# Performance work log

Measured on AMD Instinct MI355X. Metric: run time of the kernel, lower is better.

Reference implementation:

```python
import jax, jax.numpy as jnp
import numpy as np

B, N_IN, D, A, O = 2048, 2048, 1024, 4, 2048
C = 1 << A              # LUT channels per detector (sequence_length == 1)
N_LUT = D * C           # total lookup neurons


def setup_inputs() -> dict:
    key = jax.random.key(0)
    k1, k2, k3 = jax.random.split(key, 3)
    x = jax.random.normal(k1, (B, N_IN), dtype=jnp.float32)
    anchors = jax.random.randint(k2, (D, A), 0, N_IN, dtype=jnp.int64)
    # synapse weights in [min_weight, max_weight] = [0, 1]
    weights = jax.random.uniform(k3, (N_LUT, O), dtype=jnp.float32)
    return {"x": x, "anchors": anchors, "weights": weights}


def reference(x, anchors, weights):
    # Gather anchor activations: [B, D, A]
    vals = jnp.take(x, anchors, axis=1)
    # Detector bits: anchor fired iff activation > 0
    bits = (vals > 0).astype(jnp.int32)
    powers = (1 << jnp.arange(A, dtype=jnp.int32))  # [A]
    channel = jnp.sum(bits * powers, axis=-1)        # [B, D] in [0, C)
    # Lookup-neuron id per (sample, detector)
    neuron = jnp.arange(D, dtype=jnp.int32)[None, :] * C + channel  # [B, D]
    # Firing counts per lookup neuron (one fired channel per detector),
    # then accumulate each fired neuron's weight row into the output:
    # out[b] = sum_d weights[neuron[b, d]]
    counts = jnp.zeros((B, N_LUT), dtype=weights.dtype)
    counts = counts.at[jnp.arange(B)[:, None], neuron].add(1.0)
    out = counts @ weights  # [B, O]
    return out
```

## Files before the change

kernel.cpp:

```cpp
#include <hip/hip_runtime.h>
#include <hip/hip_bf16.h>


typedef __attribute__((ext_vector_type(4))) int i32x4;
typedef __attribute__((ext_vector_type(16))) int i32x16;
typedef __attribute__((ext_vector_type(4))) float f32x4;

__device__ __forceinline__ bool anchors_is_i64(const int* a) {
  int v = 0;
#pragma unroll
  for (int i = 0; i < 32; ++i) v |= a[2 * i + 1];
  return v == 0;
}

__device__ __forceinline__ int ld_anchor(const int* a, int i, bool is64) {
  return is64 ? a[2 * i] : a[i];
}

__device__ __forceinline__ i32x4 mkA(unsigned ch) {
  unsigned long long v = 1ull << ((ch << 3) & 63u);
  union { unsigned long long q[2]; i32x4 v4; } u;
  u.q[0] = (ch < 8u) ? v : 0ull;
  u.q[1] = (ch < 8u) ? 0ull : v;
  return u.v4;
}

__global__ __launch_bounds__(256) void k_bits(const float* __restrict__ x,
                                              unsigned char* __restrict__ xbT) {
  __shared__ unsigned char t[64][65];
  const int tid = threadIdx.x;
  const int tr = blockIdx.x * 64, tc = blockIdx.y * 64;
  const int c = tid & 63, r0 = tid >> 6;
#pragma unroll
  for (int j = 0; j < 16; ++j) {
    int r = r0 + j * 4;
    t[c][r] = x[(size_t)(tr + r) * 2048 + tc + c] > 0.0f ? 1 : 0;
  }
  __syncthreads();
#pragma unroll
  for (int j = 0; j < 16; ++j) {
    int n = r0 + j * 4;
    xbT[(size_t)(tc + n) * 2048 + tr + c] = t[n][c];
  }
}

__global__ __launch_bounds__(256) void k_channels3(const unsigned char* __restrict__ xbT,
                                                   const int* __restrict__ anc,
                                                   unsigned* __restrict__ chR) {
  const int s = blockIdx.x * 256 + threadIdx.x;
  const int kq = blockIdx.y;
  const bool is64 = anchors_is_i64(anc);
  unsigned word = 0;
#pragma unroll
  for (int di = 0; di < 4; ++di) {
    const int d = kq * 4 + di;
    unsigned ch = 0;
#pragma unroll
    for (int i = 0; i < 4; ++i) {
      int a = ld_anchor(anc, d * 4 + i, is64);
      ch |= (unsigned)xbT[(size_t)a * 2048 + s] << i;
    }
    word |= ch << (di * 8);
  }
  const int g = s >> 7, rf = (s >> 5) & 3, l = s & 31;
  chR[(((size_t)kq * 16 + g) * 32 + l) * 4 + rf] = word;
}

__global__ __launch_bounds__(256) void k_wfrag_i8(const float* __restrict__ W,
                                                  uint4* __restrict__ wfq) {
  const unsigned flat = blockIdx.x * 256 + threadIdx.x;
  const unsigned l = flat & 63u, nc = (flat >> 6) & 63u, kt = flat >> 12;
  const unsigned dd = 2u * kt + (l >> 5), col = nc * 32u + (l & 31u);
  const float* base = W + (size_t)(dd * 16u) * 2048u + col;
  unsigned wd[4];
#pragma unroll
  for (int wi = 0; wi < 4; ++wi) {
    unsigned v = 0;
#pragma unroll
    for (int bj = 0; bj < 4; ++bj) {
      float f = base[(size_t)(wi * 4 + bj) * 2048u];
      int q = (int)(f * 127.0f + 0.5f);
      q = q < 0 ? 0 : (q > 127 ? 127 : q);
      v |= (unsigned)q << (bj * 8);
    }
    wd[wi] = v;
  }
  uint4 o;
  o.x = wd[0]; o.y = wd[1]; o.z = wd[2]; o.w = wd[3];
  wfq[flat] = o;
}

__global__ __launch_bounds__(256, 4) void k_gemm(const uint4* __restrict__ wfq,
                                                 const unsigned* __restrict__ chR,
                                                 float* __restrict__ out) {
  constexpr int NB = 256;

  const int tid = threadIdx.x, lane = tid & 63;
  const int w = tid >> 6;
  const unsigned q = (unsigned)(lane >> 5), q8 = q << 3;

  const unsigned orig = blockIdx.x;
  const unsigned xcd = orig & 7u, slot = orig >> 3;
  const unsigned strip = xcd * 8u + (slot & 7u);
  const unsigned mBlk = slot >> 3;

  const uint4* wp0 = wfq + ((size_t)strip * 64u) + lane;
  const uint4* wp1 = wp0 + 4096;
  const unsigned g = mBlk * 2u + ((unsigned)w >> 1);
  const uint2* cp = (const uint2*)chR +
                    (((size_t)g) * 32u + (lane & 31)) * 2u + ((unsigned)w & 1u);

  i32x16 acc[2] = {};

#define MFMA_I8(a, b, c) __builtin_amdgcn_mfma_i32_32x32x32_i8((a), (b), (c), 0, 0, 0)

  uint4 b0[4], b1[4];
  uint2 cq[4];
#pragma unroll
  for (int i = 0; i < 4; ++i) {
    b0[i] = wp0[(size_t)i * 8192];
    b1[i] = wp1[(size_t)i * 8192];
    cq[i] = cp[(size_t)i * 1024];
  }

#define COMPUTE(i)                                                        \
  {                                                                       \
    const i32x4 vb0 = *(const i32x4*)&b0[i];                              \
    const i32x4 vb1 = *(const i32x4*)&b1[i];                              \
    __builtin_amdgcn_s_setprio(1);                                        \
    acc[0] = MFMA_I8(mkA((cq[i].x >> q8) & 15u), vb0, acc[0]);            \
    acc[1] = MFMA_I8(mkA((cq[i].y >> q8) & 15u), vb0, acc[1]);            \
    acc[0] = MFMA_I8(mkA((cq[i].x >> (16u + q8)) & 15u), vb1, acc[0]);    \
    acc[1] = MFMA_I8(mkA((cq[i].y >> (16u + q8)) & 15u), vb1, acc[1]);    \
    __builtin_amdgcn_s_setprio(0);                                        \
  }
#define REFILL(i, p)                                                      \
  {                                                                       \
    const int np = ((p) + 4 < NB) ? (p) + 4 : (p);                        \
    b0[i] = wp0[(size_t)np * 8192];                                       \
    b1[i] = wp1[(size_t)np * 8192];                                       \
    cq[i] = cp[(size_t)np * 1024];                                        \
  }

  for (int p = 0; p < NB; p += 4) {
    COMPUTE(0) REFILL(0, p)
    COMPUTE(1) REFILL(1, p + 1)
    COMPUTE(2) REFILL(2, p + 2)
    COMPUTE(3) REFILL(3, p + 3)
  }
#undef COMPUTE
#undef REFILL

  const float scale = 1.0f / 127.0f;
  const int c = (int)strip * 32 + (lane & 31);
  const int rowW = (int)mBlk * 256 + w * 64;
#pragma unroll
  for (int rf = 0; rf < 2; ++rf) {
    const int r0 = rowW + rf * 32 + (int)(q * 4u);
#pragma unroll
    for (int reg = 0; reg < 16; ++reg) {
      int r = r0 + (reg & 3) + 8 * (reg >> 2);
      out[(size_t)r * 2048 + c] = (float)acc[rf][reg] * scale;
    }
  }
}

__global__ __launch_bounds__(256) void k_direct(const float* __restrict__ x,
                                                const int* __restrict__ anc,
                                                const float* __restrict__ W,
                                                float* __restrict__ out) {
  __shared__ unsigned rowoff[1024];
  const int b = blockIdx.x;
  const bool is64 = anchors_is_i64(anc);
  for (int d = threadIdx.x; d < 1024; d += 256) {
    unsigned ch = 0;
#pragma unroll
    for (int i = 0; i < 4; ++i) {
      int a = ld_anchor(anc, d * 4 + i, is64);
      ch |= (x[(size_t)b * 2048 + a] > 0.0f ? 1u : 0u) << i;
    }
    rowoff[d] = (unsigned)(d * 16 + ch) * 2048u;
  }
  __syncthreads();
  f32x4 a0 = {0.f, 0.f, 0.f, 0.f}, a1 = {0.f, 0.f, 0.f, 0.f};
  const int o0 = threadIdx.x * 4, o1 = 1024 + threadIdx.x * 4;
  for (int d = 0; d < 1024; ++d) {
    unsigned ro = rowoff[d];
    a0 += *(const f32x4*)(W + ro + o0);
    a1 += *(const f32x4*)(W + ro + o1);
  }
  *(f32x4*)(out + (size_t)b * 2048 + o0) = a0;
  *(f32x4*)(out + (size_t)b * 2048 + o1) = a1;
}

extern "C" void kernel_launch(void* const* d_in, const int* in_sizes, int n_in,
                              void* d_out, int out_size, void* d_ws, size_t ws_size,
                              hipStream_t stream) {
  const float* x = (const float*)d_in[0];
  const int* anc = (const int*)d_in[1];
  const float* W = (const float*)d_in[2];
  float* out = (float*)d_out;

  const size_t CHR_BYTES = 2ull * 1024 * 1024;
  const size_t WFQ_BYTES = 32ull * 1024 * 1024;
  const size_t XBT_BYTES = 4ull * 1024 * 1024;
  const size_t BASE = CHR_BYTES + WFQ_BYTES + XBT_BYTES;

  if (ws_size < BASE) {
    k_direct<<<2048, 256, 0, stream>>>(x, anc, W, out);
    return;
  }

  unsigned* chR = (unsigned*)d_ws;
  uint4* wfq = (uint4*)((char*)d_ws + CHR_BYTES);
  unsigned char* xbT = (unsigned char*)((char*)d_ws + CHR_BYTES + WFQ_BYTES);

  k_bits<<<dim3(32, 32), 256, 0, stream>>>(x, xbT);
  k_channels3<<<dim3(8, 256), 256, 0, stream>>>(xbT, anc, chR);
  k_wfrag_i8<<<8192, 256, 0, stream>>>(W, wfq);
  k_gemm<<<512, 256, 0, stream>>>(wfq, chR, out);
}
```

Measured before the change: 102.2 us.

## Halve GEMM row tile per block and double grid size

Each GEMM wave now computes a single 32x32 accumulator tile instead of two, so a block covers 128 output rows and the grid grows to 1024 blocks. This lowers register pressure and adds more blocks for occupancy and latency hiding. The cost is that each weight fragment loaded from memory is used by half as many MFMAs, which doubles total weight-fragment traffic.

```diff
diff --git a/kernel.cpp b/kernel.cpp
--- a/kernel.cpp
+++ b/kernel.cpp
@@ -94,6 +94,7 @@
                                                  const unsigned* __restrict__ chR,
                                                  float* __restrict__ out) {
   constexpr int NB = 256;
+  constexpr int PD = 4;
 
   const int tid = threadIdx.x, lane = tid & 63;
   const int w = tid >> 6;
@@ -106,21 +107,19 @@
 
   const uint4* wp0 = wfq + ((size_t)strip * 64u) + lane;
   const uint4* wp1 = wp0 + 4096;
-  const unsigned g = mBlk * 2u + ((unsigned)w >> 1);
-  const uint2* cp = (const uint2*)chR +
-                    (((size_t)g) * 32u + (lane & 31)) * 2u + ((unsigned)w & 1u);
-
-  i32x16 acc[2] = {};
+  const unsigned* cp = chR + (((size_t)mBlk) * 32u + (lane & 31)) * 4u + (unsigned)w;
+
+  i32x16 acc = {};
 
 #define MFMA_I8(a, b, c) __builtin_amdgcn_mfma_i32_32x32x32_i8((a), (b), (c), 0, 0, 0)
 
-  uint4 b0[4], b1[4];
-  uint2 cq[4];
-#pragma unroll
-  for (int i = 0; i < 4; ++i) {
+  uint4 b0[PD], b1[PD];
+  unsigned cw[PD];
+#pragma unroll
+  for (int i = 0; i < PD; ++i) {
     b0[i] = wp0[(size_t)i * 8192];
     b1[i] = wp1[(size_t)i * 8192];
-    cq[i] = cp[(size_t)i * 1024];
+    cw[i] = cp[(size_t)i * 2048];
   }
 
 #define COMPUTE(i)                                                        \
@@ -128,21 +127,19 @@
     const i32x4 vb0 = *(const i32x4*)&b0[i];                              \
     const i32x4 vb1 = *(const i32x4*)&b1[i];                              \
     __builtin_amdgcn_s_setprio(1);                                        \
-    acc[0] = MFMA_I8(mkA((cq[i].x >> q8) & 15u), vb0, acc[0]);            \
-    acc[1] = MFMA_I8(mkA((cq[i].y >> q8) & 15u), vb0, acc[1]);            \
-    acc[0] = MFMA_I8(mkA((cq[i].x >> (16u + q8)) & 15u), vb1, acc[0]);    \
-    acc[1] = MFMA_I8(mkA((cq[i].y >> (16u + q8)) & 15u), vb1, acc[1]);    \
+    acc = MFMA_I8(mkA((cw[i] >> q8) & 15u), vb0, acc);                    \
+    acc = MFMA_I8(mkA((cw[i] >> (16u + q8)) & 15u), vb1, acc);            \
     __builtin_amdgcn_s_setprio(0);                                        \
   }
 #define REFILL(i, p)                                                      \
   {                                                                       \
-    const int np = ((p) + 4 < NB) ? (p) + 4 : (p);                        \
+    const int np = ((p) + PD < NB) ? (p) + PD : (p);                      \
     b0[i] = wp0[(size_t)np * 8192];                                       \
     b1[i] = wp1[(size_t)np * 8192];                                       \
-    cq[i] = cp[(size_t)np * 1024];                                        \
-  }
-
-  for (int p = 0; p < NB; p += 4) {
+    cw[i] = cp[(size_t)np * 2048];                                        \
+  }
+
+  for (int p = 0; p < NB; p += PD) {
     COMPUTE(0) REFILL(0, p)
     COMPUTE(1) REFILL(1, p + 1)
     COMPUTE(2) REFILL(2, p + 2)
@@ -153,15 +150,11 @@
 
   const float scale = 1.0f / 127.0f;
   const int c = (int)strip * 32 + (lane & 31);
-  const int rowW = (int)mBlk * 256 + w * 64;
-#pragma unroll
-  for (int rf = 0; rf < 2; ++rf) {
-    const int r0 = rowW + rf * 32 + (int)(q * 4u);
-#pragma unroll
-    for (int reg = 0; reg < 16; ++reg) {
-      int r = r0 + (reg & 3) + 8 * (reg >> 2);
-      out[(size_t)r * 2048 + c] = (float)acc[rf][reg] * scale;
-    }
+  const int r0 = (int)mBlk * 128 + w * 32 + (int)(q * 4u);
+#pragma unroll
+  for (int reg = 0; reg < 16; ++reg) {
+    int r = r0 + (reg & 3) + 8 * (reg >> 2);
+    out[(size_t)r * 2048 + c] = (float)acc[reg] * scale;
   }
 }
 
@@ -218,5 +211,5 @@
   k_bits<<<dim3(32, 32), 256, 0, stream>>>(x, xbT);
   k_channels3<<<dim3(8, 256), 256, 0, stream>>>(xbT, anc, chR);
   k_wfrag_i8<<<8192, 256, 0, stream>>>(W, wfq);
-  k_gemm<<<512, 256, 0, stream>>>(wfq, chR, out);
-}
+  k_gemm<<<1024, 256, 0, stream>>>(wfq, chR, out);
+}
```

Measured after the change: 157.7 us. +54.4%, slower.
